# Kernel tuning notes

Hardware: AMD Instinct MI355X
Metric: run time of the kernel (lower is better)

The kernel has to match this reference:

```python
import jax, jax.numpy as jnp
import numpy as np

B = 4096      # batch
N = 32768     # total tree nodes (real + pseudo classes) = columns of x
L = 12        # tree path depth (levels)
K = 64        # siblings (brother nodes) per level, padded to fixed width
C = 16384     # number of real classes (range of y)


def setup_inputs() -> dict:
    key = jax.random.key(0)
    k1, k2, k3, k4 = jax.random.split(key, 4)
    x = jax.random.normal(k1, (B, N), dtype=jnp.float32)
    # per-level sibling index sets (constants derived from the cover tree /
    # new2index / index2brother dicts in the original module)
    brother = jax.random.randint(k2, (L, K), 0, N)
    # the true path node at each level must be one of that level's siblings
    pos = jax.random.randint(k3, (L,), 0, K)
    p_y = brother[jnp.arange(L), pos]
    y = jax.random.randint(k4, (B,), 0, C)  # class labels (path selection baked into brother/p_y)
    return {"x": x, "brother": brother, "p_y": p_y, "y": y}


def reference(x, brother, p_y, y):
    # x: [B, N] logits over all tree nodes; brother: [L, K]; p_y: [L]
    gathered = x[:, brother]                      # [B, L, K] irregular column gather
    logp = jax.nn.log_softmax(gathered, axis=-1)  # per-level softmax over siblings
    # label = first position of the path node within its sibling set (torch nonzero()[0])
    labels = jnp.argmax(brother == p_y[:, None], axis=-1)          # [L]
    sel = jnp.take_along_axis(logp, labels[None, :, None], axis=2)[..., 0]  # [B, L]
    # CrossEntropyLoss = mean over batch of NLL, summed across tree levels
    return (-sel).mean(axis=0).sum()
```

## Files before the change

kernel.cpp:

```cpp
#include <hip/hip_runtime.h>

#define BB 4096
#define NN 32768
#define LL 12
#define KK 64

constexpr int CHUNK = 8;
constexpr int NWAVES = LL * (BB / CHUNK);
constexpr int WPB = 4;
constexpr int NBLOCKS = NWAVES / WPB;

__global__ __launch_bounds__(256) void hsm_partial(
    const float* __restrict__ x,
    const int* __restrict__ brother,
    const int* __restrict__ p_y,
    float* __restrict__ partials) {

    const int wave_in_block = threadIdx.x >> 6;
    const int lane = threadIdx.x & 63;
    const int wid = blockIdx.x * WPB + wave_in_block;

    const int chunk = wid / LL;
    const int l = wid - chunk * LL;
    const int b0 = chunk * CHUNK;

    const int col = brother[l * KK + lane];
    const int py = p_y[l];
    const int label = __ffsll(__ballot(col == py)) - 1;

    const float* __restrict__ xp = x + (size_t)b0 * NN + col;

    float v[CHUNK];
    #pragma unroll
    for (int bi = 0; bi < CHUNK; ++bi)
        v[bi] = xp[(size_t)bi * NN];

    float local = 0.f;
    #pragma unroll
    for (int bi = 0; bi < CHUNK; ++bi) {
        float mx = v[bi];
        #pragma unroll
        for (int o = 32; o > 0; o >>= 1) mx = fmaxf(mx, __shfl_xor(mx, o));
        float s = __expf(v[bi] - mx);
        #pragma unroll
        for (int o = 32; o > 0; o >>= 1) s += __shfl_xor(s, o);
        const float lse = mx + __logf(s);
        local += lse - __shfl(v[bi], label);
    }

    __shared__ float red[WPB];
    if (lane == 0) red[wave_in_block] = local;
    __syncthreads();
    if (threadIdx.x == 0) {
        float s = 0.f;
        #pragma unroll
        for (int i = 0; i < WPB; ++i) s += red[i];
        partials[blockIdx.x] = s;
    }
}

__global__ __launch_bounds__(256) void hsm_final(
    const float* __restrict__ partials, float* __restrict__ out, int n) {
    float s = 0.f;
    for (int i = threadIdx.x; i < n; i += 256) s += partials[i];
    #pragma unroll
    for (int o = 32; o > 0; o >>= 1) s += __shfl_xor(s, o);
    __shared__ float red[4];
    const int wave = threadIdx.x >> 6, lane = threadIdx.x & 63;
    if (lane == 0) red[wave] = s;
    __syncthreads();
    if (threadIdx.x == 0) {
        out[0] = (red[0] + red[1] + red[2] + red[3]) / (float)BB;
    }
}

extern "C" void kernel_launch(void* const* d_in, const int* in_sizes, int n_in,
                              void* d_out, int out_size, void* d_ws, size_t ws_size,
                              hipStream_t stream) {
    const float* x       = (const float*)d_in[0];
    const int*   brother = (const int*)d_in[1];
    const int*   p_y     = (const int*)d_in[2];
    float* out      = (float*)d_out;
    float* partials = (float*)d_ws;

    hsm_partial<<<NBLOCKS, 256, 0, stream>>>(x, brother, p_y, partials);
    hsm_final<<<1, 256, 0, stream>>>(partials, out, NBLOCKS);
}
```

Baseline: 635.3 us.

## Stream full rows of x coalesced and scatter sibling columns into LDS

The per-level scattered column gather is replaced by coalesced float4 streaming of every row of x. A precomputed column-to-slot map, built by a new single-block kernel, tells each thread which loaded values to scatter into a shared-memory buffer of the 768 sibling logits. Duplicate columns are resolved through a dup index. After that the per-level log-softmax runs from LDS. This trades roughly 400 MB of poorly coalesced gather traffic for a full 512 MB sequential read, plus map reads and branchy LDS stores, and adds an extra kernel launch.

Measured after the change: 713.0 us. 12.2% more time.

```diff
diff --git a/kernel.cpp b/kernel.cpp
--- a/kernel.cpp
+++ b/kernel.cpp
@@ -4,73 +4,129 @@
 #define NN 32768
 #define LL 12
 #define KK 64
+#define SS (LL * KK)
 
-constexpr int CHUNK = 8;
-constexpr int NWAVES = LL * (BB / CHUNK);
-constexpr int WPB = 4;
-constexpr int NBLOCKS = NWAVES / WPB;
+constexpr int TPB    = 256;
+constexpr int NBLK   = 2048;
+constexpr int RPB    = BB / NBLK;
+constexpr int F4_ROW = NN / 4;
+constexpr int F4_THR = F4_ROW / TPB;
+constexpr int UNROLL = 8;
 
-__global__ __launch_bounds__(256) void hsm_partial(
+constexpr size_t WS_MAP  = 0;
+constexpr size_t WS_DUP  = 65536;
+constexpr size_t WS_PART = 69632;
+
+__global__ __launch_bounds__(256) void build_map(
+    const int* __restrict__ brother,
+    short* __restrict__ map,
+    short* __restrict__ dup) {
+    for (int i = threadIdx.x; i < NN * 2 / 8; i += TPB)
+        ((unsigned long long*)map)[i] = 0ULL;
+    __syncthreads();
+    for (int s = threadIdx.x; s < SS; s += TPB)
+        map[brother[s]] = (short)(s + 1);
+    __syncthreads();
+    for (int s = threadIdx.x; s < SS; s += TPB)
+        dup[s] = (short)(map[brother[s]] - 1);
+}
+
+__global__ __launch_bounds__(256) void hsm_stream(
     const float* __restrict__ x,
     const int* __restrict__ brother,
     const int* __restrict__ p_y,
+    const short* __restrict__ map,
+    const short* __restrict__ dupv,
     float* __restrict__ partials) {
 
-    const int wave_in_block = threadIdx.x >> 6;
+    __shared__ float gath[SS];
+
+    const int w    = threadIdx.x >> 6;
     const int lane = threadIdx.x & 63;
-    const int wid = blockIdx.x * WPB + wave_in_block;
 
-    const int chunk = wid / LL;
-    const int l = wid - chunk * LL;
-    const int b0 = chunk * CHUNK;
+    int dslot[3], label[3];
+    #pragma unroll
+    for (int j = 0; j < 3; ++j) {
+        const int l   = w + 4 * j;
+        const int col = brother[l * KK + lane];
+        const int py  = p_y[l];
+        label[j] = __ffsll(__ballot(col == py)) - 1;
+        dslot[j] = dupv[l * KK + lane];
+    }
+    float acc[3] = {0.f, 0.f, 0.f};
 
-    const int col = brother[l * KK + lane];
-    const int py = p_y[l];
-    const int label = __ffsll(__ballot(col == py)) - 1;
+    const uint2* mp = (const uint2*)map;
 
-    const float* __restrict__ xp = x + (size_t)b0 * NN + col;
+    for (int r = 0; r < RPB; ++r) {
+        const int b = blockIdx.x * RPB + r;
+        const float4* __restrict__ xr = (const float4*)(x + (size_t)b * NN);
 
-    float v[CHUNK];
-    #pragma unroll
-    for (int bi = 0; bi < CHUNK; ++bi)
-        v[bi] = xp[(size_t)bi * NN];
+        #pragma unroll 1
+        for (int base = 0; base < F4_THR; base += UNROLL) {
+            float4 v[UNROLL];
+            uint2  m[UNROLL];
+            #pragma unroll
+            for (int u = 0; u < UNROLL; ++u) {
+                const int fi = (base + u) * TPB + threadIdx.x;
+                v[u] = xr[fi];
+                m[u] = mp[fi];
+            }
+            #pragma unroll
+            for (int u = 0; u < UNROLL; ++u) {
+                if (m[u].x | m[u].y) {
+                    const int s0 = (int)(short)(m[u].x & 0xffff);
+                    const int s1 = (int)(short)(m[u].x >> 16);
+                    const int s2 = (int)(short)(m[u].y & 0xffff);
+                    const int s3 = (int)(short)(m[u].y >> 16);
+                    if (s0 > 0) gath[s0 - 1] = v[u].x;
+                    if (s1 > 0) gath[s1 - 1] = v[u].y;
+                    if (s2 > 0) gath[s2 - 1] = v[u].z;
+                    if (s3 > 0) gath[s3 - 1] = v[u].w;
+                }
+            }
+        }
+        __syncthreads();
 
-    float local = 0.f;
-    #pragma unroll
-    for (int bi = 0; bi < CHUNK; ++bi) {
-        float mx = v[bi];
         #pragma unroll
-        for (int o = 32; o > 0; o >>= 1) mx = fmaxf(mx, __shfl_xor(mx, o));
-        float s = __expf(v[bi] - mx);
-        #pragma unroll
-        for (int o = 32; o > 0; o >>= 1) s += __shfl_xor(s, o);
-        const float lse = mx + __logf(s);
-        local += lse - __shfl(v[bi], label);
+        for (int j = 0; j < 3; ++j) {
+            const float vv = gath[dslot[j]];
+            float mx = vv;
+            #pragma unroll
+            for (int o = 32; o > 0; o >>= 1) mx = fmaxf(mx, __shfl_xor(mx, o));
+            float s = __expf(vv - mx);
+            #pragma unroll
+            for (int o = 32; o > 0; o >>= 1) s += __shfl_xor(s, o);
+            acc[j] += mx + __logf(s) - __shfl(vv, label[j]);
+        }
+        __syncthreads();
     }
 
-    __shared__ float red[WPB];
-    if (lane == 0) red[wave_in_block] = local;
-    __syncthreads();
-    if (threadIdx.x == 0) {
-        float s = 0.f;
+    if (lane == 0) {
         #pragma unroll
-        for (int i = 0; i < WPB; ++i) s += red[i];
-        partials[blockIdx.x] = s;
+        for (int j = 0; j < 3; ++j)
+            partials[(w + 4 * j) * NBLK + blockIdx.x] = acc[j];
     }
 }
 
 __global__ __launch_bounds__(256) void hsm_final(
-    const float* __restrict__ partials, float* __restrict__ out, int n) {
-    float s = 0.f;
-    for (int i = threadIdx.x; i < n; i += 256) s += partials[i];
+    const float* __restrict__ partials, float* __restrict__ out) {
+    const int w = threadIdx.x >> 6, lane = threadIdx.x & 63;
+    __shared__ float red[LL];
     #pragma unroll
-    for (int o = 32; o > 0; o >>= 1) s += __shfl_xor(s, o);
-    __shared__ float red[4];
-    const int wave = threadIdx.x >> 6, lane = threadIdx.x & 63;
-    if (lane == 0) red[wave] = s;
+    for (int j = 0; j < 3; ++j) {
+        const int l = w + 4 * j;
+        float s = 0.f;
+        for (int i = lane; i < NBLK; i += 64) s += partials[l * NBLK + i];
+        #pragma unroll
+        for (int o = 32; o > 0; o >>= 1) s += __shfl_xor(s, o);
+        if (lane == 0) red[l] = s / (float)BB;
+    }
     __syncthreads();
     if (threadIdx.x == 0) {
-        out[0] = (red[0] + red[1] + red[2] + red[3]) / (float)BB;
+        float t = 0.f;
+        #pragma unroll
+        for (int i = 0; i < LL; ++i) t += red[i];
+        out[0] = t;
     }
 }
 
@@ -80,9 +136,14 @@
     const float* x       = (const float*)d_in[0];
     const int*   brother = (const int*)d_in[1];
     const int*   p_y     = (const int*)d_in[2];
-    float* out      = (float*)d_out;
-    float* partials = (float*)d_ws;
+    float* out = (float*)d_out;
+    char*  ws  = (char*)d_ws;
 
-    hsm_partial<<<NBLOCKS, 256, 0, stream>>>(x, brother, p_y, partials);
-    hsm_final<<<1, 256, 0, stream>>>(partials, out, NBLOCKS);
+    short* map      = (short*)(ws + WS_MAP);
+    short* dup      = (short*)(ws + WS_DUP);
+    float* partials = (float*)(ws + WS_PART);
+
+    build_map<<<1, TPB, 0, stream>>>(brother, map, dup);
+    hsm_stream<<<NBLK, TPB, 0, stream>>>(x, brother, p_y, map, dup, partials);
+    hsm_final<<<1, 256, 0, stream>>>(partials, out);
 }
```
